# Kernel optimization log

Hardware: AMD Instinct MI355X
Metric: run time of the kernel (lower is better)

The kernel has to match this reference:

```python
import jax, jax.numpy as jnp
import numpy as np
import math

HEAD_DIM = 128
NUM_Q_HEAD = 32
NUM_KV_HEAD = 8
WINDOW = 512
CAP = 30.0
CLIP_LO, CLIP_HI = -0.03, 1.03
EPS = 1e-5
SCALE = 1.0 / math.sqrt(HEAD_DIM)
B, S = 2, 2048


def group_rms_norm(x, w, group_size, eps):
    # x: [B, S, hidden]; normalize each contiguous group of size group_size
    Bx, Sx, H = x.shape
    ng = H // group_size
    xg = x.reshape(Bx, Sx, ng, group_size)
    inv = jax.lax.rsqrt(jnp.mean(xg * xg, axis=-1, keepdims=True) + eps)
    return (xg * inv).reshape(Bx, Sx, H) * w


def setup_inputs() -> dict:
    key = jax.random.key(0)
    kq, kk, kv, kw1, kw2 = jax.random.split(key, 5)
    q = jax.random.normal(kq, (B, S, NUM_Q_HEAD, HEAD_DIM), dtype=jnp.float32)
    k = jax.random.normal(kk, (B, S, NUM_KV_HEAD, HEAD_DIM), dtype=jnp.float32)
    v = jax.random.normal(kv, (B, S, NUM_KV_HEAD, HEAD_DIM), dtype=jnp.float32)
    # GroupRMSNorm weights, init uniform in (-1, 1)
    q_norm_w = jax.random.uniform(kw1, (NUM_Q_HEAD * HEAD_DIM,), dtype=jnp.float32, minval=-1.0, maxval=1.0)
    kv_norm_w = jax.random.uniform(kw2, (NUM_KV_HEAD * HEAD_DIM,), dtype=jnp.float32, minval=-1.0, maxval=1.0)
    return {"q": q, "k": k, "v": v, "q_norm_w": q_norm_w, "kv_norm_w": kv_norm_w}


def reference(q, k, v, q_norm_w, kv_norm_w):
    Bq, Sq, Hq, D = q.shape
    Sk = k.shape[1]
    # QK GroupRMSNorm over flattened hidden dim, group_size = head_dim
    qn = group_rms_norm(q.reshape(Bq, Sq, Hq * D), q_norm_w, HEAD_DIM, EPS).reshape(q.shape)
    kn = group_rms_norm(k.reshape(Bq, Sk, NUM_KV_HEAD * D), kv_norm_w, HEAD_DIM, EPS).reshape(k.shape)
    # GQA: repeat_interleave kv heads along head axis
    rep = Hq // NUM_KV_HEAD
    kr = jnp.repeat(kn, rep, axis=2)  # [B, Sk, Hq, D]
    vr = jnp.repeat(v, rep, axis=2)
    # scores: [B, Hq, Sq, Sk]
    scores = jnp.einsum("bqhd,bkhd->bhqk", qn, kr) * SCALE
    scores = CAP * jnp.tanh(scores / CAP)  # softmax capping
    # sliding-window + causal mask: allowed iff i - WINDOW <= j <= i (offset = Sk - Sq = 0)
    offset = Sk - Sq
    i = jnp.arange(Sq)[:, None] + offset
    j = jnp.arange(Sk)[None, :]
    allowed = (j <= i) & (j >= i - WINDOW)
    scores = jnp.where(allowed, scores, -jnp.inf)
    probs = jax.nn.softmax(scores, axis=-1)
    probs = jnp.nan_to_num(probs, nan=0.0)
    # softmax clipping
    probs = jnp.clip((CLIP_HI - CLIP_LO) * probs + CLIP_LO, 0.0, 1.0)
    out = jnp.einsum("bhqk,bkhd->bqhd", probs, vr)
    return out
```

## Files before the change

### kernel.cpp

```cpp
#include <hip/hip_runtime.h>

#define SEQ 2048
#define DD 128
#define HQ 32
#define HKV 8
#define WIN 512

typedef unsigned short u16;
typedef unsigned int u32;
typedef __attribute__((ext_vector_type(8))) short bf16x8;
typedef __attribute__((ext_vector_type(4))) float f32x4;
typedef __attribute__((ext_vector_type(2))) float f32x2;

#define SBAR() asm volatile("s_barrier" ::: "memory")
#define WAITV0() asm volatile("s_waitcnt vmcnt(0)" ::: "memory")

__device__ __forceinline__ u16 f2bf(float f) {
  u32 u = __builtin_bit_cast(u32, f);
  u += 0x7FFFu + ((u >> 16) & 1u);
  return (u16)(u >> 16);
}

__device__ __forceinline__ void gl16(const void* g, void* l) {
  __builtin_amdgcn_global_load_lds(
      (const __attribute__((address_space(1))) void*)g,
      (__attribute__((address_space(3))) void*)l, 16, 0, 0);
}

__device__ __forceinline__ u32 cvtpk(float lo, float hi) {
  u32 r;
  asm("v_cvt_pk_bf16_f32 %0, %1, %2" : "=v"(r) : "v"(lo), "v"(hi));
  return r;
}

__device__ __forceinline__ f32x2 pk_mul(f32x2 a, f32x2 b) {
  f32x2 d;
  asm("v_pk_mul_f32 %0, %1, %2" : "=v"(d) : "v"(a), "v"(b));
  return d;
}
__device__ __forceinline__ f32x2 pk_fma(f32x2 a, f32x2 b, f32x2 c) {
  f32x2 d;
  asm("v_pk_fma_f32 %0, %1, %2, %3" : "=v"(d) : "v"(a), "v"(b), "v"(c));
  return d;
}
__device__ __forceinline__ f32x2 pk_add(f32x2 a, f32x2 b) {
  f32x2 d;
  asm("v_pk_add_f32 %0, %1, %2" : "=v"(d) : "v"(a), "v"(b));
  return d;
}

__device__ __forceinline__ f32x2 score2(f32x2 x, f32x2 vL2E, f32x2 vmCE, f32x2 vmCTL) {
  f32x2 x2 = pk_mul(x, x);
  f32x2 a1 = pk_fma(x, vL2E, vmCE);
  f32x2 b1 = pk_mul(x2, vmCTL);
  return pk_fma(b1, x, a1);
}

__device__ __forceinline__ f32x2 unpk(u32 wv) {
  f32x2 r;
  r[0] = __builtin_bit_cast(float, wv << 16);
  r[1] = __builtin_bit_cast(float, wv & 0xFFFF0000u);
  return r;
}

__device__ __forceinline__ void norm_body(
    const float* __restrict__ x, const float* __restrict__ w,
    u16* __restrict__ o, int hshift, int blk, int tid) {
  const int lane = tid & 63;
  const int wv = tid >> 6;
  const int sub = lane >> 5;
  const int l5 = lane & 31;
  const int rid = blk * 8 + wv * 2 + sub;
  const int H = 1 << hshift;
  const int hh = rid & (H - 1);
  const int s = (rid >> hshift) & (SEQ - 1);
  const int b = rid >> (hshift + 11);
  const float4 xv = *(reinterpret_cast<const float4*>(x + (size_t)rid * DD) + l5);
  float ssq = xv.x * xv.x + xv.y * xv.y + xv.z * xv.z + xv.w * xv.w;
  ssq += __shfl_xor(ssq, 1);
  ssq += __shfl_xor(ssq, 2);
  ssq += __shfl_xor(ssq, 4);
  ssq += __shfl_xor(ssq, 8);
  ssq += __shfl_xor(ssq, 16);
  const float inv = rsqrtf(ssq * (1.0f / 128.0f) + 1e-5f);
  const float4 wv4 = *(reinterpret_cast<const float4*>(w + hh * DD) + l5);
  const u16 o0 = f2bf(xv.x * inv * wv4.x);
  const u16 o1 = f2bf(xv.y * inv * wv4.y);
  const u16 o2 = f2bf(xv.z * inv * wv4.z);
  const u16 o3 = f2bf(xv.w * inv * wv4.w);
  const size_t oo = (((size_t)b * H + hh) * SEQ + s) * DD + l5 * 4;
  uint2 pk;
  pk.x = (u32)o0 | ((u32)o1 << 16);
  pk.y = (u32)o2 | ((u32)o3 << 16);
  *reinterpret_cast<uint2*>(o + oo) = pk;
}

__device__ __forceinline__ void transv_body(
    const float* __restrict__ v, u16* __restrict__ vt, int bid, int t) {
  const int st = bid & 31;
  const int h = (bid >> 5) & 7;
  const int b = bid >> 8;
  const int sbase = st * 64;
  const int d = t & 127;
  const int sch = (t >> 7) * 32;
  const size_t oo = (((size_t)(b * HKV + h)) * DD + d) * SEQ + sbase + sch;
#pragma unroll
  for (int q8 = 0; q8 < 4; ++q8) {
    uint4 o;
    u32 c[4];
#pragma unroll
    for (int p = 0; p < 4; ++p) {
      const int ss0 = q8 * 8 + p * 2;
      const int s0 = sbase + sch + ss0;
      const float a0 = v[((size_t)(b * SEQ + s0) * HKV + h) * DD + d];
      const float a1 = v[((size_t)(b * SEQ + s0 + 1) * HKV + h) * DD + d];
      c[p] = (u32)f2bf(a0) | ((u32)f2bf(a1) << 16);
    }
    o.x = c[0]; o.y = c[1]; o.z = c[2]; o.w = c[3];
    *reinterpret_cast<uint4*>(vt + oo + q8 * 8) = o;
  }
}

__global__ void __launch_bounds__(256) prep_kernel(
    const float* __restrict__ k, const float* __restrict__ v,
    const float* __restrict__ kw, u16* __restrict__ kn, u16* __restrict__ vt) {
  const int blk = blockIdx.x;
  const int tid = threadIdx.x;
  if (blk < 4096) {
    norm_body(k, kw, kn, 3, blk, tid);
  } else {
    transv_body(v, vt, blk - 4096, tid);
  }
}

__global__ void __launch_bounds__(256, 3) attn_kernel(
    const float* __restrict__ q32, const float* __restrict__ qw,
    const u16* __restrict__ kn, const u16* __restrict__ vt,
    float* __restrict__ out) {
  __shared__ char smem[32768];
  const int tid = threadIdx.x;
  const int w = tid >> 6;
  const int lane = tid & 63;
  const int c = lane & 15;
  const int g = lane >> 4;

  const int p = blockIdx.x;
  const int bid = ((p & 7) << 8) + (p >> 3);
  const int qt = (bid & 127) ^ 127;
  const int hk = (bid >> 7) & 7;
  const int b = bid >> 10;
  const int i0 = qt * 16;
  const int h = hk * 4 + w;

  const u16* kbp = kn + (size_t)(b * HKV + hk) * SEQ * DD;
  const u16* vbp = vt + (size_t)(b * HKV + hk) * DD * SEQ;

  int ks = i0 - WIN;
  ks = (ks < 0) ? 0 : (ks & ~63);
  const int ntl = (i0 + 16 - ks + 63) >> 6;

  auto stageK = [&](int kb, int bufoff) {
    char* dst = smem + bufoff;
#pragma unroll
    for (int ci = 0; ci < 4; ++ci) {
      const int call = w * 4 + ci;
      const int row = call * 4 + g;
      const int ch = c ^ (row & 7);
      gl16(kbp + (size_t)(kb + row) * DD + ch * 8, dst + call * 1024);
    }
  };
  auto stageV = [&](int kb, int bufoff) {
    char* dst = smem + bufoff;
#pragma unroll
    for (int ci = 0; ci < 4; ++ci) {
      const int call = w * 4 + ci;
      const int vrow = call * 8 + (lane >> 3);
      const int vch = (lane & 7) ^ (vrow & 7);
      gl16(vbp + (size_t)vrow * SEQ + kb + vch * 8, dst + call * 1024);
    }
  };

  const float* qf = q32 + (((size_t)b * SEQ + i0 + c) * HQ + h) * DD;
  const float* wf = qw + h * DD;
  f32x4 qx[4][2];
#pragma unroll
  for (int kt = 0; kt < 4; ++kt) {
    qx[kt][0] = __builtin_nontemporal_load(
        reinterpret_cast<const f32x4*>(qf + kt * 32 + g * 8));
    qx[kt][1] = __builtin_nontemporal_load(
        reinterpret_cast<const f32x4*>(qf + kt * 32 + g * 8 + 4));
  }
  f32x4 qwv[4][2];
#pragma unroll
  for (int kt = 0; kt < 4; ++kt) {
    qwv[kt][0] = *reinterpret_cast<const f32x4*>(wf + kt * 32 + g * 8);
    qwv[kt][1] = *reinterpret_cast<const f32x4*>(wf + kt * 32 + g * 8 + 4);
  }

  stageK(ks, 0);

  union AQ { bf16x8 v; u32 w4[4]; };
  AQ aq[4];
  {
    float ss = 0.0f;
#pragma unroll
    for (int kt = 0; kt < 4; ++kt) {
#pragma unroll
      for (int half = 0; half < 2; ++half) {
        const f32x4 a = qx[kt][half];
        ss = fmaf(a[0], a[0], ss); ss = fmaf(a[1], a[1], ss);
        ss = fmaf(a[2], a[2], ss); ss = fmaf(a[3], a[3], ss);
      }
    }
    ss += __shfl_xor(ss, 16);
    ss += __shfl_xor(ss, 32);
    const float inv = rsqrtf(ss * (1.0f / 128.0f) + 1e-5f) * 0.08838834764831845f;
#pragma unroll
    for (int kt = 0; kt < 4; ++kt) {
      const f32x4 a0 = qx[kt][0];
      const f32x4 a1 = qx[kt][1];
      const f32x4 w0 = qwv[kt][0];
      const f32x4 w1 = qwv[kt][1];
      aq[kt].w4[0] = cvtpk(a0[0] * inv * w0[0], a0[1] * inv * w0[1]);
      aq[kt].w4[1] = cvtpk(a0[2] * inv * w0[2], a0[3] * inv * w0[3]);
      aq[kt].w4[2] = cvtpk(a1[0] * inv * w1[0], a1[1] * inv * w1[1]);
      aq[kt].w4[3] = cvtpk(a1[2] * inv * w1[2], a1[3] * inv * w1[3]);
    }
  }

  const f32x2 vL2E = {1.44269504088896f, 1.44269504088896f};
  const f32x2 vmCE = {-43.2808512266689f, -43.2808512266689f};
  const f32x2 vmCTL = {-5.343315e-4f, -5.343315e-4f};

  u32 ebuf[9][8];
  f32x2 lsum2 = {0.0f, 0.0f};

#pragma unroll
  for (int t = 0; t < 9; ++t) {
    if (t >= ntl) continue;
    const int kb = ks + t * 64;
    WAITV0();
    SBAR();
    if (t + 1 < ntl) {
      stageK(kb + 64, ((t + 1) & 1) << 14);
    } else {
      stageV(ks, (ntl & 1) << 14);
    }

    const char* kbuf = smem + ((t & 1) << 14);
    f32x4 sc[4] = {};
    __builtin_amdgcn_s_setprio(1);
#pragma unroll
    for (int nt = 0; nt < 4; ++nt) {
      const int jb = kb + nt * 16;
      if (jb > i0 + 15 || jb + 15 < i0 - WIN) continue;
      const int row = nt * 16 + c;
      const int sw = row & 7;
      const char* base = kbuf + row * 256;
#pragma unroll
      for (int kt = 0; kt < 4; ++kt) {
        const bf16x8 bk = *reinterpret_cast<const bf16x8*>(base + (((kt * 4 + g) ^ sw) << 4));
        sc[nt] = __builtin_amdgcn_mfma_f32_16x16x32_bf16(bk, aq[kt].v, sc[nt], 0, 0, 0);
      }
    }
    __builtin_amdgcn_s_setprio(0);

#pragma unroll
    for (int nt = 0; nt < 4; ++nt) {
      const int jb = kb + nt * 16;
      if (jb > i0 + 15 || jb + 15 < i0 - WIN) {
        ebuf[t][nt * 2] = 0;
        ebuf[t][nt * 2 + 1] = 0;
        continue;
      }
      const bool needmask = (jb + 15 > i0) || (jb < i0 + 15 - WIN);
      f32x2 lo = __builtin_shufflevector(sc[nt], sc[nt], 0, 1);
      f32x2 hi = __builtin_shufflevector(sc[nt], sc[nt], 2, 3);
      const f32x2 a0 = score2(lo, vL2E, vmCE, vmCTL);
      const f32x2 a1 = score2(hi, vL2E, vmCE, vmCTL);
      float e0 = __builtin_amdgcn_exp2f(a0[0]);
      float e1 = __builtin_amdgcn_exp2f(a0[1]);
      float e2 = __builtin_amdgcn_exp2f(a1[0]);
      float e3 = __builtin_amdgcn_exp2f(a1[1]);
      if (needmask) {
        const int difg = i0 + c - jb - g * 4;
        e0 = ((u32)(difg - 0) <= WIN) ? e0 : 0.0f;
        e1 = ((u32)(difg - 1) <= WIN) ? e1 : 0.0f;
        e2 = ((u32)(difg - 2) <= WIN) ? e2 : 0.0f;
        e3 = ((u32)(difg - 3) <= WIN) ? e3 : 0.0f;
      }
      ebuf[t][nt * 2] = cvtpk(e0, e1);
      ebuf[t][nt * 2 + 1] = cvtpk(e2, e3);
      const f32x2 eA = {e0, e1};
      const f32x2 eB = {e2, e3};
      lsum2 = pk_add(lsum2, pk_add(eA, eB));
    }
  }

  float l = lsum2[0] + lsum2[1];
  l += __shfl_xor(l, 16);
  l += __shfl_xor(l, 32);
  const float ar = 1.06f / l;
  const f32x2 var2 = {ar, ar};
  const f32x2 vm003 = {-0.03f, -0.03f};

  f32x4 acc[8] = {};

#pragma unroll
  for (int t = 0; t < 9; ++t) {
    if (t >= ntl) continue;
    const int kb = ks + t * 64;
    WAITV0();
    SBAR();
    if (t + 1 < ntl) stageV(kb + 64, (((t + 1) + ntl) & 1) << 14);
    const char* ldsV = smem + (((t + ntl) & 1) << 14);

#pragma unroll
    for (int k2 = 0; k2 < 2; ++k2) {
      const int jb2 = kb + k2 * 32;
      if (jb2 > i0 + 15 || jb2 + 31 < i0 - WIN) continue;

      u32 cw[4];
#pragma unroll
      for (int u = 0; u < 4; ++u) {
        const f32x2 ef = unpk(ebuf[t][k2 * 4 + u]);
        const f32x2 pr = pk_fma(ef, var2, vm003);
        cw[u] = cvtpk(__builtin_amdgcn_fmed3f(pr[0], 0.0f, 1.0f),
                      __builtin_amdgcn_fmed3f(pr[1], 0.0f, 1.0f));
      }

      const u32 nz = (cw[0] | cw[1]) | (cw[2] | cw[3]);
      if (!__any(nz != 0)) continue;

      union PU { bf16x8 v; u32 w4[4]; };
      PU pf;
      {
        u32 x0 = cw[0], y0 = cw[2];
        asm("v_permlane32_swap_b32 %0, %1" : "+v"(x0), "+v"(y0));
        asm("v_permlane16_swap_b32 %0, %1" : "+v"(x0), "+v"(y0));
        u32 x1 = cw[1], y1 = cw[3];
        asm("v_permlane32_swap_b32 %0, %1" : "+v"(x1), "+v"(y1));
        asm("v_permlane16_swap_b32 %0, %1" : "+v"(x1), "+v"(y1));
        pf.w4[0] = x0;
        pf.w4[1] = x1;
        pf.w4[2] = y0;
        pf.w4[3] = y1;
      }

      __builtin_amdgcn_s_setprio(1);
#pragma unroll
      for (int dt = 0; dt < 8; ++dt) {
        const int rv = dt * 16 + c;
        const bf16x8 bv = *reinterpret_cast<const bf16x8*>(
            ldsV + rv * 128 + (((k2 * 4 + g) ^ (rv & 7)) << 4));
        acc[dt] = __builtin_amdgcn_mfma_f32_16x16x32_bf16(pf.v, bv, acc[dt], 0, 0, 0);
      }
      __builtin_amdgcn_s_setprio(0);
    }
  }

#pragma unroll
  for (int r = 0; r < 4; ++r) {
    const int i = i0 + g * 4 + r;
    float* op = out + (((size_t)b * SEQ + i) * HQ + h) * DD + c;
#pragma unroll
    for (int dt = 0; dt < 8; ++dt)
      __builtin_nontemporal_store(acc[dt][r], op + dt * 16);
  }
}

extern "C" void kernel_launch(void* const* d_in, const int* in_sizes, int n_in,
                              void* d_out, int out_size, void* d_ws, size_t ws_size,
                              hipStream_t stream) {
  const float* q = (const float*)d_in[0];
  const float* k = (const float*)d_in[1];
  const float* v = (const float*)d_in[2];
  const float* qw = (const float*)d_in[3];
  const float* kw = (const float*)d_in[4];
  float* out = (float*)d_out;

  u16* kn = (u16*)d_ws;
  u16* vt = kn + (size_t)2 * HKV * SEQ * DD;

  prep_kernel<<<4608, 256, 0, stream>>>(k, v, kw, kn, vt);
  attn_kernel<<<2048, 256, 0, stream>>>(q, qw, kn, vt, out);
}
```

Before: 82.82 us.

## Triple-buffer K staging and skip V tiles whose clipped probabilities are all zero

The K-tile pipeline moves from double to triple buffering, prefetching two tiles ahead with a partial vmcnt wait so the loads overlap more compute. After the row sums are known, a per-tile mask is built from a threshold equal to the point where clipped probabilities become zero. It is combined across waves through LDS, and V staging plus the PV MFMAs run only for tiles that can contribute. This removes global loads and MFMA work for tiles whose probabilities all clip to zero. In exchange LDS grows to about 48KB, which may lower occupancy from 3 blocks per CU, and an extra barrier and mask pass are added.

```diff
diff --git a/kernel.cpp b/kernel.cpp
--- a/kernel.cpp
+++ b/kernel.cpp
@@ -8,12 +8,15 @@
 
 typedef unsigned short u16;
 typedef unsigned int u32;
+typedef unsigned long long u64;
 typedef __attribute__((ext_vector_type(8))) short bf16x8;
 typedef __attribute__((ext_vector_type(4))) float f32x4;
 typedef __attribute__((ext_vector_type(2))) float f32x2;
 
 #define SBAR() asm volatile("s_barrier" ::: "memory")
 #define WAITV0() asm volatile("s_waitcnt vmcnt(0)" ::: "memory")
+#define WAITV4() asm volatile("s_waitcnt vmcnt(4)" ::: "memory")
+#define WAITLGKM0() asm volatile("s_waitcnt lgkmcnt(0)" ::: "memory")
 
 __device__ __forceinline__ u16 f2bf(float f) {
   u32 u = __builtin_bit_cast(u32, f);
@@ -137,7 +140,7 @@
     const float* __restrict__ q32, const float* __restrict__ qw,
     const u16* __restrict__ kn, const u16* __restrict__ vt,
     float* __restrict__ out) {
-  __shared__ char smem[32768];
+  __shared__ char smem[49168];
   const int tid = threadIdx.x;
   const int w = tid >> 6;
   const int lane = tid & 63;
@@ -198,6 +201,7 @@
   }
 
   stageK(ks, 0);
+  if (ntl > 1) stageK(ks + 64, 16384);
 
   union AQ { bf16x8 v; u32 w4[4]; };
   AQ aq[4];
@@ -239,15 +243,11 @@
   for (int t = 0; t < 9; ++t) {
     if (t >= ntl) continue;
     const int kb = ks + t * 64;
-    WAITV0();
+    if (t + 1 < ntl) { WAITV4(); } else { WAITV0(); }
     SBAR();
-    if (t + 1 < ntl) {
-      stageK(kb + 64, ((t + 1) & 1) << 14);
-    } else {
-      stageV(ks, (ntl & 1) << 14);
-    }
-
-    const char* kbuf = smem + ((t & 1) << 14);
+    if (t + 2 < ntl) stageK(kb + 128, ((t + 2) % 3) << 14);
+
+    const char* kbuf = smem + ((t % 3) << 14);
     f32x4 sc[4] = {};
     __builtin_amdgcn_s_setprio(1);
 #pragma unroll
@@ -301,19 +301,55 @@
   l += __shfl_xor(l, 16);
   l += __shfl_xor(l, 32);
   const float ar = 1.06f / l;
+  const float thr = 0.0283018868f * l;
+
+  u32 m9w = 0;
+#pragma unroll
+  for (int t = 0; t < 9; ++t) {
+    if (t >= ntl) continue;
+    bool nz = false;
+#pragma unroll
+    for (int u = 0; u < 8; ++u) {
+      const f32x2 ef = unpk(ebuf[t][u]);
+      nz = nz || (ef[0] > thr) || (ef[1] > thr);
+    }
+    if (__any(nz)) m9w |= 1u << t;
+  }
+
+  u32* mk = reinterpret_cast<u32*>(smem + 49152);
+  mk[w] = m9w;
+  WAITLGKM0();
+  SBAR();
+  const u32 m9 = mk[0] | mk[1] | mk[2] | mk[3];
+
+  u64 nxtp = 0xFULL << 36;
+  {
+    int nx = 15;
+#pragma unroll
+    for (int t = 8; t >= 0; --t) {
+      if (m9 & (1u << t)) nx = t;
+      nxtp |= (u64)nx << (4 * t);
+    }
+  }
+  const int f0 = (int)(nxtp & 15);
+  if (f0 < 9) stageV(ks + f0 * 64, 0);
+
   const f32x2 var2 = {ar, ar};
   const f32x2 vm003 = {-0.03f, -0.03f};
 
   f32x4 acc[8] = {};
+  int vi = 0;
 
 #pragma unroll
   for (int t = 0; t < 9; ++t) {
     if (t >= ntl) continue;
+    if (!(m9 & (1u << t))) continue;
     const int kb = ks + t * 64;
     WAITV0();
     SBAR();
-    if (t + 1 < ntl) stageV(kb + 64, (((t + 1) + ntl) & 1) << 14);
-    const char* ldsV = smem + (((t + ntl) & 1) << 14);
+    const int nx2 = (int)((nxtp >> (4 * (t + 1))) & 15);
+    if (nx2 < 9) stageV(ks + nx2 * 64, ((vi + 1) & 1) << 14);
+    const char* ldsV = smem + ((vi & 1) << 14);
 
 #pragma unroll
     for (int k2 = 0; k2 < 2; ++k2) {
@@ -357,6 +393,7 @@
       }
       __builtin_amdgcn_s_setprio(0);
     }
+    ++vi;
   }
 
 #pragma unroll
```

Result: faster. 75.67 us (median of 2 runs) (-8.6%).
